# Optimization experiments

Hardware: AMD Instinct MI355X
Metric: run time of the kernel (lower is better)

Reference implementation:

```python
import jax, jax.numpy as jnp
import numpy as np

N = 50000        # nodes
E = 800000       # edges (avg degree 16)
OBS = 128        # observation_dim
HID = 64         # hidden_dim (per head)
H1 = 4           # heads in conv1
ACT = 32         # action_dim
NEG_SLOPE = 0.2  # GATv2 default negative_slope


def setup_inputs() -> dict:
    key = jax.random.key(0)
    ks = jax.random.split(key, 10)
    s = 0.05
    x = jax.random.normal(ks[0], (N, OBS), jnp.float32)
    edge_index = jax.random.randint(ks[1], (2, E), 0, N, dtype=jnp.int32)
    # conv1: GATv2Conv(OBS -> HID, heads=4, concat=True)
    W1l = jax.random.normal(ks[2], (OBS, H1 * HID), jnp.float32) * s  # lin_l (source)
    W1r = jax.random.normal(ks[3], (OBS, H1 * HID), jnp.float32) * s  # lin_r (target)
    att1 = jax.random.normal(ks[4], (H1, HID), jnp.float32) * s
    b1 = jnp.zeros((H1 * HID,), jnp.float32)
    # conv2: GATv2Conv(H1*HID -> ACT, heads=1, concat=False)
    W2l = jax.random.normal(ks[5], (H1 * HID, ACT), jnp.float32) * s
    W2r = jax.random.normal(ks[6], (H1 * HID, ACT), jnp.float32) * s
    att2 = jax.random.normal(ks[7], (1, ACT), jnp.float32) * s
    b2 = jnp.zeros((ACT,), jnp.float32)
    return {"x": x, "edge_index": edge_index, "W1l": W1l, "W1r": W1r,
            "att1": att1, "b1": b1, "W2l": W2l, "W2r": W2r,
            "att2": att2, "b2": b2}


def gatv2_layer(x, Wl, Wr, att, bias, src, dst, heads, out_ch, concat):
    """PyG GATv2Conv (add_self_loops=False, share_weights=False)."""
    n = x.shape[0]
    xl = (x @ Wl).reshape(n, heads, out_ch)  # source transform
    xr = (x @ Wr).reshape(n, heads, out_ch)  # target transform
    e = xl[src] + xr[dst]                    # [E, H, C] gathered messages
    g = jnp.where(e > 0, e, NEG_SLOPE * e)   # LeakyReLU
    logits = jnp.einsum('ehc,hc->eh', g, att)  # [E, H]
    # segment softmax over incoming edges of each destination node
    m = jax.ops.segment_max(logits, dst, num_segments=n)      # [N, H]
    ex = jnp.exp(logits - m[dst])
    denom = jax.ops.segment_sum(ex, dst, num_segments=n)      # [N, H]
    alpha = ex / denom[dst]                                   # [E, H]
    out = jax.ops.segment_sum(xl[src] * alpha[:, :, None], dst, num_segments=n)
    out = out.reshape(n, heads * out_ch) if concat else out.mean(axis=1)
    return out + bias


def reference(x, edge_index, W1l, W1r, att1, b1, W2l, W2r, att2, b2):
    src, dst = edge_index[0], edge_index[1]
    h = jax.nn.relu(gatv2_layer(x, W1l, W1r, att1, b1, src, dst, H1, HID, True))
    out = gatv2_layer(h, W2l, W2r, att2, b2, src, dst, 1, ACT, False)
    return out
```

## Files before the change

### kernel.cpp

```cpp
#include <hip/hip_runtime.h>
#include <hip/hip_bf16.h>
#include <math.h>


#define OBS 128
#define HID 64
#define H1 4
#define C1 256
#define ACT 32
#define PAD 128
#define NEG_SLOPE 0.2f
#define LOG2E 1.4426950408889634f

typedef __attribute__((ext_vector_type(2))) _Float16 h2;
typedef __attribute__((ext_vector_type(8))) _Float16 half8;
typedef __attribute__((ext_vector_type(4))) float f32x4;

__device__ inline h2 bc_h2(unsigned u) { return __builtin_bit_cast(h2, u); }
__device__ inline unsigned bc_u(h2 v) { return __builtin_bit_cast(unsigned, v); }
__device__ inline h2 lrelu2(h2 e) {
  const h2 k = {(_Float16)NEG_SLOPE, (_Float16)NEG_SLOPE};
  return __builtin_elementwise_max(e, e * k);
}

__global__ void prep0(const float* __restrict__ W1l, const float* __restrict__ W1r,
                      const float* __restrict__ W2l, const float* __restrict__ W2r,
                      _Float16* __restrict__ W1t, _Float16* __restrict__ W2t,
                      int* __restrict__ cursor, int N) {
  int i = blockIdx.x * 256 + threadIdx.x;
  if (i < N) cursor[i] = 0;
  if (i < 512 * 128) {
    int n = i >> 7, k = i & 127;
    float v = (n < C1) ? W1l[k * C1 + n] : W1r[k * C1 + (n - C1)];
    W1t[i] = (_Float16)v;
  }
  int j = i - 512 * 128;
  if (j >= 0 && j < 64 * 256) {
    int n = j >> 8, c = j & 255;
    float v = (n < ACT) ? W2l[c * ACT + n] : W2r[c * ACT + (n - ACT)];
    W2t[j] = (_Float16)v;
  }
}

__global__ __launch_bounds__(256) void gemm1_csr(
    const float* __restrict__ xf,
    const _Float16* __restrict__ W1t,
    _Float16* __restrict__ XLh,
    _Float16* __restrict__ XRh,
    int M,
    const int* __restrict__ src, const int* __restrict__ dst,
    int* __restrict__ cursor, unsigned short* __restrict__ esrc_p,
    int E, int gemmBlocks) {
  const int LDK = 136;
  __shared__ _Float16 As[128 * 136];
  __shared__ _Float16 Bs[128 * 136];

  if ((int)blockIdx.x >= gemmBlocks) {
    int e = ((int)blockIdx.x - gemmBlocks) * 256 + threadIdx.x;
    if (e < E) {
      int d = dst[e];
      int slot = atomicAdd(&cursor[d], 1);
      if (slot < PAD) esrc_p[((size_t)d << 7) + slot] = (unsigned short)src[e];
    }
    return;
  }

  const int tid = threadIdx.x;
  const int lane = tid & 63;
  const int wid = tid >> 6;
  const int wm = (wid & 1) * 64, wn = (wid >> 1) * 64;
  const int rowBase = blockIdx.x * 128;
  const int l15 = lane & 15, lq = lane >> 4;

#pragma unroll
  for (int cc = 0; cc < 8; ++cc) {
    int q = cc * 256 + tid;
    int r = q >> 4;
    int kc = (q & 15) * 8;
    int grow = rowBase + r;
    float4 f0 = make_float4(0.f, 0.f, 0.f, 0.f), f1 = f0;
    if (grow < M) {
      f0 = *(const float4*)(xf + (size_t)grow * 128 + kc);
      f1 = *(const float4*)(xf + (size_t)grow * 128 + kc + 4);
    }
    h2 p0 = {(_Float16)f0.x, (_Float16)f0.y};
    h2 p1 = {(_Float16)f0.z, (_Float16)f0.w};
    h2 p2 = {(_Float16)f1.x, (_Float16)f1.y};
    h2 p3 = {(_Float16)f1.z, (_Float16)f1.w};
    *(int4*)(As + r * LDK + kc) = make_int4(bc_u(p0), bc_u(p1), bc_u(p2), bc_u(p3));
  }
#pragma unroll
  for (int cc = 0; cc < 8; ++cc) {
    int q = cc * 256 + tid;
    int r = q >> 4;
    int kc = (q & 15) * 8;
    *(int4*)(Bs + r * LDK + kc) = *(const int4*)(W1t + (size_t)r * 128 + kc);
  }
  __syncthreads();

  for (int cb = 0; cb < 4; ++cb) {
    f32x4 acc[4][4];
#pragma unroll
    for (int i = 0; i < 4; ++i)
#pragma unroll
      for (int j = 0; j < 4; ++j) acc[i][j] = (f32x4){0.f, 0.f, 0.f, 0.f};

#pragma unroll
    for (int ks = 0; ks < 4; ++ks) {
      half8 af[4], bf[4];
#pragma unroll
      for (int t = 0; t < 4; ++t) {
        af[t] = *(const half8*)(As + (wm + t * 16 + l15) * LDK + ks * 32 + lq * 8);
        bf[t] = *(const half8*)(Bs + (wn + t * 16 + l15) * LDK + ks * 32 + lq * 8);
      }
#pragma unroll
      for (int mt = 0; mt < 4; ++mt)
#pragma unroll
        for (int nt = 0; nt < 4; ++nt)
          acc[mt][nt] = __builtin_amdgcn_mfma_f32_16x16x32_f16(
              af[mt], bf[nt], acc[mt][nt], 0, 0, 0);
    }

    _Float16* outp = (cb < 2) ? XLh : XRh;
    int colBase = (cb & 1) * 128;
#pragma unroll
    for (int mt = 0; mt < 4; ++mt) {
#pragma unroll
      for (int r = 0; r < 4; ++r) {
        int row = rowBase + wm + mt * 16 + lq * 4 + r;
        if (row >= M) continue;
#pragma unroll
        for (int nt = 0; nt < 4; ++nt) {
          int col = colBase + wn + nt * 16 + l15;
          outp[(size_t)row * C1 + col] = (_Float16)acc[mt][nt][r];
        }
      }
    }

    if (cb < 3) {
      __syncthreads();
#pragma unroll
      for (int cc = 0; cc < 8; ++cc) {
        int q = cc * 256 + tid;
        int r = q >> 4;
        int kc = (q & 15) * 8;
        *(int4*)(Bs + r * LDK + kc) =
            *(const int4*)(W1t + (size_t)((cb + 1) * 128 + r) * 128 + kc);
      }
      __syncthreads();
    }
  }
}

__global__ __launch_bounds__(256) void gemm_mfma2(
    const _Float16* __restrict__ Hh,
    const _Float16* __restrict__ W2t,
    _Float16* __restrict__ H2h,
    int M) {
  const int LDK = 136;
  __shared__ _Float16 As[128 * 136];
  __shared__ _Float16 Bs[64 * 136];
  const int tid = threadIdx.x;
  const int lane = tid & 63;
  const int wid = tid >> 6;
  const int wm = (wid & 1) * 64, wn = (wid >> 1) * 32;
  const int rowBase = blockIdx.x * 128;

  f32x4 acc[4][2];
#pragma unroll
  for (int i = 0; i < 4; ++i)
#pragma unroll
    for (int j = 0; j < 2; ++j) acc[i][j] = (f32x4){0.f, 0.f, 0.f, 0.f};

  const int l15 = lane & 15, lq = lane >> 4;

  for (int kb = 0; kb < 256; kb += 128) {
#pragma unroll
    for (int cc = 0; cc < 8; ++cc) {
      int q = cc * 256 + tid;
      int r = q >> 4;
      int kc = (q & 15) * 8;
      int grow = rowBase + r;
      int4 av = make_int4(0, 0, 0, 0);
      if (grow < M) av = *(const int4*)(Hh + (size_t)grow * 256 + kb + kc);
      *(int4*)(As + r * LDK + kc) = av;
    }
#pragma unroll
    for (int cc = 0; cc < 4; ++cc) {
      int q = cc * 256 + tid;
      int r = q >> 4;
      int kc = (q & 15) * 8;
      *(int4*)(Bs + r * LDK + kc) = *(const int4*)(W2t + (size_t)r * 256 + kb + kc);
    }
    __syncthreads();

#pragma unroll
    for (int ks = 0; ks < 4; ++ks) {
      half8 af[4], bf[2];
#pragma unroll
      for (int t = 0; t < 4; ++t)
        af[t] = *(const half8*)(As + (wm + t * 16 + l15) * LDK + ks * 32 + lq * 8);
#pragma unroll
      for (int t = 0; t < 2; ++t)
        bf[t] = *(const half8*)(Bs + (wn + t * 16 + l15) * LDK + ks * 32 + lq * 8);
#pragma unroll
      for (int mt = 0; mt < 4; ++mt)
#pragma unroll
        for (int nt = 0; nt < 2; ++nt)
          acc[mt][nt] = __builtin_amdgcn_mfma_f32_16x16x32_f16(
              af[mt], bf[nt], acc[mt][nt], 0, 0, 0);
    }
    __syncthreads();
  }

#pragma unroll
  for (int mt = 0; mt < 4; ++mt) {
#pragma unroll
    for (int r = 0; r < 4; ++r) {
      int row = rowBase + wm + mt * 16 + lq * 4 + r;
      if (row >= M) continue;
#pragma unroll
      for (int nt = 0; nt < 2; ++nt) {
        int col = wn + nt * 16 + l15;
        H2h[(size_t)row * 64 + col] = (_Float16)acc[mt][nt][r];
      }
    }
  }
}

__global__ __launch_bounds__(256) void agg1(const _Float16* __restrict__ XLh,
                                            const _Float16* XRh,
                                            const float* __restrict__ att1,
                                            const float* __restrict__ b1,
                                            const int* __restrict__ degp,
                                            const unsigned short* __restrict__ esrc_p,
                                            _Float16* Hh, int n_nodes) {
  int wave = threadIdx.x >> 6;
  int lane = threadIdx.x & 63;
  int n = blockIdx.x * 4 + wave;
  if (n >= n_nodes) return;
  int sl = lane & 31;
  int half = lane >> 5;
  int c8 = sl * 8;

  const char* XLb = (const char*)XLh + c8 * 2;
  int4 xru = *(const int4*)((const char*)XRh + ((size_t)n << 9) + c8 * 2);
  h2 xr[4] = {bc_h2(xru.x), bc_h2(xru.y), bc_h2(xru.z), bc_h2(xru.w)};
  const float* ap = att1 + (c8 >> 6) * HID + (c8 & 63);
  float4 a0 = *(const float4*)ap;
  float4 a1 = *(const float4*)(ap + 4);
  h2 av[4] = {{(_Float16)(a0.x * LOG2E), (_Float16)(a0.y * LOG2E)},
              {(_Float16)(a0.z * LOG2E), (_Float16)(a0.w * LOG2E)},
              {(_Float16)(a1.x * LOG2E), (_Float16)(a1.y * LOG2E)},
              {(_Float16)(a1.z * LOG2E), (_Float16)(a1.w * LOG2E)}};

  int d = min(degp[n], PAD);
  const unsigned short* ep = esrc_p + ((size_t)n << 7);
  float l = 0.f;
  h2 acc[4];
#pragma unroll
  for (int k = 0; k < 4; ++k) acc[k] = (h2){(_Float16)0.f, (_Float16)0.f};

  int base = 0;
  for (; base + 16 <= d; base += 16) {
    int4 u[8];
#pragma unroll
    for (int t = 0; t < 8; ++t) {
      int s = ep[base + 2 * t + half];
      u[t] = *(const int4*)(XLb + ((size_t)s << 9));
    }
    float c[8];
#pragma unroll
    for (int t = 0; t < 8; ++t) {
      h2 xa = bc_h2(u[t].x), xb = bc_h2(u[t].y), xc = bc_h2(u[t].z), xd = bc_h2(u[t].w);
      float cc = __builtin_amdgcn_fdot2(lrelu2(xa + xr[0]), av[0], 0.f, false);
      cc = __builtin_amdgcn_fdot2(lrelu2(xb + xr[1]), av[1], cc, false);
      cc = __builtin_amdgcn_fdot2(lrelu2(xc + xr[2]), av[2], cc, false);
      cc = __builtin_amdgcn_fdot2(lrelu2(xd + xr[3]), av[3], cc, false);
      c[t] = cc;
    }
#pragma unroll
    for (int t = 0; t < 8; ++t) {
      c[t] += __shfl_xor(c[t], 1);
      c[t] += __shfl_xor(c[t], 2);
      c[t] += __shfl_xor(c[t], 4);
    }
#pragma unroll
    for (int t = 0; t < 8; ++t) {
      float p = __builtin_amdgcn_exp2f(c[t]);
      l += p;
      _Float16 ph = (_Float16)p;
      h2 w = {ph, ph};
      acc[0] = acc[0] + w * bc_h2(u[t].x);
      acc[1] = acc[1] + w * bc_h2(u[t].y);
      acc[2] = acc[2] + w * bc_h2(u[t].z);
      acc[3] = acc[3] + w * bc_h2(u[t].w);
    }
  }
  for (; base + 4 <= d; base += 4) {
    int s0 = ep[base + half];
    int s1 = ep[base + 2 + half];
    int4 u0 = *(const int4*)(XLb + ((size_t)s0 << 9));
    int4 u1 = *(const int4*)(XLb + ((size_t)s1 << 9));
    h2 x0[4] = {bc_h2(u0.x), bc_h2(u0.y), bc_h2(u0.z), bc_h2(u0.w)};
    h2 x1[4] = {bc_h2(u1.x), bc_h2(u1.y), bc_h2(u1.z), bc_h2(u1.w)};
    float c0 = 0.f, c1 = 0.f;
#pragma unroll
    for (int k = 0; k < 4; ++k) {
      c0 = __builtin_amdgcn_fdot2(lrelu2(x0[k] + xr[k]), av[k], c0, false);
      c1 = __builtin_amdgcn_fdot2(lrelu2(x1[k] + xr[k]), av[k], c1, false);
    }
    c0 += __shfl_xor(c0, 1); c1 += __shfl_xor(c1, 1);
    c0 += __shfl_xor(c0, 2); c1 += __shfl_xor(c1, 2);
    c0 += __shfl_xor(c0, 4); c1 += __shfl_xor(c1, 4);
    float p0 = __builtin_amdgcn_exp2f(c0);
    float p1 = __builtin_amdgcn_exp2f(c1);
    l += p0 + p1;
    _Float16 q0 = (_Float16)p0, q1 = (_Float16)p1;
    h2 w0 = {q0, q0}, w1 = {q1, q1};
#pragma unroll
    for (int k = 0; k < 4; ++k) acc[k] = acc[k] + w0 * x0[k] + w1 * x1[k];
  }
  if (base < d) {
    int e0 = base + half, e1 = base + 2 + half;
    bool v0 = e0 < d, v1 = e1 < d;
    int s0 = ep[v0 ? e0 : 0];
    int s1 = ep[v1 ? e1 : 0];
    int4 u0 = *(const int4*)(XLb + ((size_t)s0 << 9));
    int4 u1 = *(const int4*)(XLb + ((size_t)s1 << 9));
    h2 x0[4] = {bc_h2(u0.x), bc_h2(u0.y), bc_h2(u0.z), bc_h2(u0.w)};
    h2 x1[4] = {bc_h2(u1.x), bc_h2(u1.y), bc_h2(u1.z), bc_h2(u1.w)};
    float c0 = 0.f, c1 = 0.f;
#pragma unroll
    for (int k = 0; k < 4; ++k) {
      c0 = __builtin_amdgcn_fdot2(lrelu2(x0[k] + xr[k]), av[k], c0, false);
      c1 = __builtin_amdgcn_fdot2(lrelu2(x1[k] + xr[k]), av[k], c1, false);
    }
    c0 += __shfl_xor(c0, 1); c1 += __shfl_xor(c1, 1);
    c0 += __shfl_xor(c0, 2); c1 += __shfl_xor(c1, 2);
    c0 += __shfl_xor(c0, 4); c1 += __shfl_xor(c1, 4);
    float p0 = v0 ? __builtin_amdgcn_exp2f(c0) : 0.f;
    float p1 = v1 ? __builtin_amdgcn_exp2f(c1) : 0.f;
    l += p0 + p1;
    _Float16 q0 = (_Float16)p0, q1 = (_Float16)p1;
    h2 w0 = {q0, q0}, w1 = {q1, q1};
#pragma unroll
    for (int k = 0; k < 4; ++k) acc[k] = acc[k] + w0 * x0[k] + w1 * x1[k];
  }

  l += __shfl_xor(l, 32);
#pragma unroll
  for (int k = 0; k < 4; ++k) {
    unsigned o = __shfl_xor((int)bc_u(acc[k]), 32);
    acc[k] = acc[k] + bc_h2(o);
  }

  float inv = (d > 0) ? 1.f / l : 0.f;
  if (half == 0) {
    float4 b0 = *(const float4*)(b1 + c8);
    float4 b3 = *(const float4*)(b1 + c8 + 4);
    float o0 = fmaxf((float)acc[0][0] * inv + b0.x, 0.f);
    float o1 = fmaxf((float)acc[0][1] * inv + b0.y, 0.f);
    float o2 = fmaxf((float)acc[1][0] * inv + b0.z, 0.f);
    float o3 = fmaxf((float)acc[1][1] * inv + b0.w, 0.f);
    float o4 = fmaxf((float)acc[2][0] * inv + b3.x, 0.f);
    float o5 = fmaxf((float)acc[2][1] * inv + b3.y, 0.f);
    float o6 = fmaxf((float)acc[3][0] * inv + b3.z, 0.f);
    float o7 = fmaxf((float)acc[3][1] * inv + b3.w, 0.f);
    h2 q0 = {(_Float16)o0, (_Float16)o1};
    h2 q1 = {(_Float16)o2, (_Float16)o3};
    h2 q2 = {(_Float16)o4, (_Float16)o5};
    h2 q3 = {(_Float16)o6, (_Float16)o7};
    *(int4*)((char*)Hh + ((size_t)n << 9) + c8 * 2) =
        make_int4(bc_u(q0), bc_u(q1), bc_u(q2), bc_u(q3));
  }
}

__global__ __launch_bounds__(256) void agg2(const _Float16* __restrict__ H2h,
                                            const float* __restrict__ att2,
                                            const float* __restrict__ b2,
                                            const int* __restrict__ degp,
                                            const unsigned short* __restrict__ esrc_p,
                                            float* __restrict__ out, int n_nodes) {
  int wave = threadIdx.x >> 6;
  int lane = threadIdx.x & 63;
  int n = blockIdx.x * 4 + wave;
  if (n >= n_nodes) return;
  int g = lane >> 3;
  int j = lane & 7;
  int c4 = j * 4;

  const char* Hb = (const char*)H2h + c4 * 2;
  uint2 hru = *(const uint2*)((const char*)H2h + ((size_t)n << 7) + 64 + c4 * 2);
  h2 hr0 = bc_h2(hru.x), hr1 = bc_h2(hru.y);
  float4 af = *(const float4*)(att2 + c4);
  h2 a0 = {(_Float16)(af.x * LOG2E), (_Float16)(af.y * LOG2E)};
  h2 a1 = {(_Float16)(af.z * LOG2E), (_Float16)(af.w * LOG2E)};

  int d = min(degp[n], PAD);
  const unsigned short* ep = esrc_p + ((size_t)n << 7);
  float l = 0.f;
  h2 acc0 = {(_Float16)0.f, (_Float16)0.f}, acc1 = acc0;

  int base = 0;
  for (; base + 16 <= d; base += 16) {
    int s0 = ep[base + g];
    int s1 = ep[base + 8 + g];
    uint2 u0 = *(const uint2*)(Hb + ((size_t)s0 << 7));
    uint2 u1 = *(const uint2*)(Hb + ((size_t)s1 << 7));
    h2 h00 = bc_h2(u0.x), h01 = bc_h2(u0.y);
    h2 h10 = bc_h2(u1.x), h11 = bc_h2(u1.y);
    float c0 = __builtin_amdgcn_fdot2(lrelu2(h00 + hr0), a0,
               __builtin_amdgcn_fdot2(lrelu2(h01 + hr1), a1, 0.f, false), false);
    float c1 = __builtin_amdgcn_fdot2(lrelu2(h10 + hr0), a0,
               __builtin_amdgcn_fdot2(lrelu2(h11 + hr1), a1, 0.f, false), false);
    c0 += __shfl_xor(c0, 1); c1 += __shfl_xor(c1, 1);
    c0 += __shfl_xor(c0, 2); c1 += __shfl_xor(c1, 2);
    c0 += __shfl_xor(c0, 4); c1 += __shfl_xor(c1, 4);
    float p0 = __builtin_amdgcn_exp2f(c0);
    float p1 = __builtin_amdgcn_exp2f(c1);
    l += p0 + p1;
    _Float16 q0 = (_Float16)p0, q1 = (_Float16)p1;
    h2 w0 = {q0, q0}, w1 = {q1, q1};
    acc0 = acc0 + w0 * h00 + w1 * h10;
    acc1 = acc1 + w0 * h01 + w1 * h11;
  }
  for (; base + 8 <= d; base += 8) {
    int s = ep[base + g];
    uint2 u = *(const uint2*)(Hb + ((size_t)s << 7));
    h2 h0 = bc_h2(u.x), h1 = bc_h2(u.y);
    float c = __builtin_amdgcn_fdot2(lrelu2(h0 + hr0), a0,
              __builtin_amdgcn_fdot2(lrelu2(h1 + hr1), a1, 0.f, false), false);
    c += __shfl_xor(c, 1);
    c += __shfl_xor(c, 2);
    c += __shfl_xor(c, 4);
    float p = __builtin_amdgcn_exp2f(c);
    l += p;
    _Float16 ph = (_Float16)p;
    h2 p2 = {ph, ph};
    acc0 = acc0 + p2 * h0;
    acc1 = acc1 + p2 * h1;
  }
  if (base < d) {
    int e = base + g;
    bool v = e < d;
    int s = ep[v ? e : 0];
    uint2 u = *(const uint2*)(Hb + ((size_t)s << 7));
    h2 h0 = bc_h2(u.x), h1 = bc_h2(u.y);
    float c = __builtin_amdgcn_fdot2(lrelu2(h0 + hr0), a0,
              __builtin_amdgcn_fdot2(lrelu2(h1 + hr1), a1, 0.f, false), false);
    c += __shfl_xor(c, 1);
    c += __shfl_xor(c, 2);
    c += __shfl_xor(c, 4);
    float p = v ? __builtin_amdgcn_exp2f(c) : 0.f;
    l += p;
    _Float16 ph = (_Float16)p;
    h2 p2 = {ph, ph};
    acc0 = acc0 + p2 * h0;
    acc1 = acc1 + p2 * h1;
  }

#pragma unroll
  for (int o = 8; o < 64; o <<= 1) {
    l += __shfl_xor(l, o);
    acc0 = acc0 + bc_h2((unsigned)__shfl_xor((int)bc_u(acc0), o));
    acc1 = acc1 + bc_h2((unsigned)__shfl_xor((int)bc_u(acc1), o));
  }

  float inv = (d > 0) ? 1.f / l : 0.f;
  if (g == 0) {
    float4 bb = *(const float4*)(b2 + c4);
    float4 o;
    o.x = (float)acc0[0] * inv + bb.x;
    o.y = (float)acc0[1] * inv + bb.y;
    o.z = (float)acc1[0] * inv + bb.z;
    o.w = (float)acc1[1] * inv + bb.w;
    *(float4*)(out + (size_t)n * ACT + c4) = o;
  }
}

extern "C" void kernel_launch(void* const* d_in, const int* in_sizes, int n_in,
                              void* d_out, int out_size, void* d_ws, size_t ws_size,
                              hipStream_t stream) {
  (void)n_in; (void)out_size; (void)ws_size;
  const float* x    = (const float*)d_in[0];
  const int*   ei   = (const int*)d_in[1];
  const float* W1l  = (const float*)d_in[2];
  const float* W1r  = (const float*)d_in[3];
  const float* att1 = (const float*)d_in[4];
  const float* b1   = (const float*)d_in[5];
  const float* W2l  = (const float*)d_in[6];
  const float* W2r  = (const float*)d_in[7];
  const float* att2 = (const float*)d_in[8];
  const float* b2   = (const float*)d_in[9];
  float* out = (float*)d_out;

  const int N = in_sizes[0] / OBS;
  const int E = in_sizes[1] / 2;
  const int* src = ei;
  const int* dst = ei + E;

  _Float16* XLh = (_Float16*)d_ws;
  _Float16* XRh = XLh + (size_t)N * C1;
  _Float16* W1t = XRh + (size_t)N * C1;
  _Float16* W2t = W1t + 512 * 128;
  int* cursor   = (int*)(W2t + 64 * 256);
  unsigned short* esrc_p = (unsigned short*)(cursor + N);
  _Float16* Hh  = XRh;
  _Float16* H2h = XLh;

  dim3 b256(256);
  int csrBlocks = (E + 255) / 256;
  int gemmBlocks = (N + 127) / 128;
  int prepBlocks = (512 * 128 + 64 * 256 + 255) / 256;

  prep0<<<prepBlocks, b256, 0, stream>>>(W1l, W1r, W2l, W2r, W1t, W2t, cursor, N);
  gemm1_csr<<<gemmBlocks + csrBlocks, b256, 0, stream>>>(
      x, W1t, XLh, XRh, N, src, dst, cursor, esrc_p, E, gemmBlocks);
  agg1<<<(N + 3) / 4, b256, 0, stream>>>(XLh, XRh, att1, b1, cursor, esrc_p, Hh, N);
  gemm_mfma2<<<gemmBlocks, b256, 0, stream>>>(Hh, W2t, H2h, N);
  agg2<<<(N + 3) / 4, b256, 0, stream>>>(H2h, att2, b2, cursor, esrc_p, out, N);
}
```

Before: 226.2 us.

## Build padded CSR via two-pass bucketed scatter instead of global atomics

Replaces the per-edge global atomicAdd on per-node cursors with a two-level bucket sort: edges are first scattered into 256-node buckets using shared-memory counts and one global atomic per bucket per block, then each bucket builds its padded neighbor lists with shared-memory atomics. This is meant to cut global atomic contention and scattered 2-byte writes. It also stops overlapping CSR construction with gemm1, adds two kernel launches, and places the sorted buffer at the start of the workspace, where it aliases XLh before gemm1 writes it. A bucket holding more than 8192 edges would overflow its region.

```diff
diff --git a/kernel.cpp b/kernel.cpp
--- a/kernel.cpp
+++ b/kernel.cpp
@@ -11,6 +11,8 @@
 #define PAD 128
 #define NEG_SLOPE 0.2f
 #define LOG2E 1.4426950408889634f
+#define SB 512
+#define CAP 8192
 
 typedef __attribute__((ext_vector_type(2))) _Float16 h2;
 typedef __attribute__((ext_vector_type(8))) _Float16 half8;
@@ -26,9 +28,9 @@
 __global__ void prep0(const float* __restrict__ W1l, const float* __restrict__ W1r,
                       const float* __restrict__ W2l, const float* __restrict__ W2r,
                       _Float16* __restrict__ W1t, _Float16* __restrict__ W2t,
-                      int* __restrict__ cursor, int N) {
+                      unsigned* __restrict__ bucketCursor) {
   int i = blockIdx.x * 256 + threadIdx.x;
-  if (i < N) cursor[i] = 0;
+  if (i < 256) bucketCursor[i] = 0;
   if (i < 512 * 128) {
     int n = i >> 7, k = i & 127;
     float v = (n < C1) ? W1l[k * C1 + n] : W1r[k * C1 + (n - C1)];
@@ -42,28 +44,70 @@
   }
 }
 
-__global__ __launch_bounds__(256) void gemm1_csr(
+__global__ __launch_bounds__(256) void scat2_k(const int* __restrict__ src,
+                                               const int* __restrict__ dst,
+                                               unsigned* __restrict__ bucketCursor,
+                                               unsigned* __restrict__ sorted,
+                                               int E, int epb) {
+  __shared__ unsigned cnt[256];
+  __shared__ unsigned lbase[256];
+  __shared__ unsigned lrank[256];
+  int t = threadIdx.x;
+  cnt[t] = 0;
+  lrank[t] = 0;
+  __syncthreads();
+  int beg = blockIdx.x * epb;
+  int end = beg + epb;
+  if (end > E) end = E;
+  for (int e = beg + t; e < end; e += 256)
+    atomicAdd(&cnt[dst[e] >> 8], 1u);
+  __syncthreads();
+  unsigned c = cnt[t];
+  lbase[t] = c ? atomicAdd(&bucketCursor[t], c) : 0u;
+  __syncthreads();
+  for (int e = beg + t; e < end; e += 256) {
+    int d = dst[e];
+    int sv = src[e];
+    int b = d >> 8;
+    unsigned r = atomicAdd(&lrank[b], 1u);
+    sorted[(size_t)b * CAP + lbase[b] + r] =
+        ((unsigned)(d & 255) << 16) | (unsigned)sv;
+  }
+}
+
+__global__ __launch_bounds__(256) void bcsr_k(const unsigned* __restrict__ sorted,
+                                              const unsigned* __restrict__ bucketCursor,
+                                              unsigned short* __restrict__ esrc_p,
+                                              int* __restrict__ cursor, int N) {
+  __shared__ unsigned cnt2[256];
+  int b = blockIdx.x;
+  int t = threadIdx.x;
+  cnt2[t] = 0;
+  __syncthreads();
+  unsigned total = bucketCursor[b];
+  const unsigned* sp = sorted + (size_t)b * CAP;
+  for (unsigned e = t; e < total; e += 256) {
+    unsigned u = sp[e];
+    unsigned dl = u >> 16;
+    unsigned slot = atomicAdd(&cnt2[dl], 1u);
+    if (slot < PAD)
+      esrc_p[((size_t)((b << 8) + (int)dl) << 7) + slot] =
+          (unsigned short)(u & 0xFFFFu);
+  }
+  __syncthreads();
+  int node = (b << 8) + t;
+  if (node < N) cursor[node] = (int)cnt2[t];
+}
+
+__global__ __launch_bounds__(256) void gemm1(
     const float* __restrict__ xf,
     const _Float16* __restrict__ W1t,
     _Float16* __restrict__ XLh,
     _Float16* __restrict__ XRh,
-    int M,
-    const int* __restrict__ src, const int* __restrict__ dst,
-    int* __restrict__ cursor, unsigned short* __restrict__ esrc_p,
-    int E, int gemmBlocks) {
+    int M) {
   const int LDK = 136;
   __shared__ _Float16 As[128 * 136];
   __shared__ _Float16 Bs[128 * 136];
-
-  if ((int)blockIdx.x >= gemmBlocks) {
-    int e = ((int)blockIdx.x - gemmBlocks) * 256 + threadIdx.x;
-    if (e < E) {
-      int d = dst[e];
-      int slot = atomicAdd(&cursor[d], 1);
-      if (slot < PAD) esrc_p[((size_t)d << 7) + slot] = (unsigned short)src[e];
-    }
-    return;
-  }
 
   const int tid = threadIdx.x;
   const int lane = tid & 63;
@@ -509,14 +553,19 @@
   _Float16* Hh  = XRh;
   _Float16* H2h = XLh;
 
+  unsigned* sortedW = (unsigned*)d_ws;
+  unsigned* bcur    = sortedW + 256 * CAP;
+
   dim3 b256(256);
-  int csrBlocks = (E + 255) / 256;
   int gemmBlocks = (N + 127) / 128;
   int prepBlocks = (512 * 128 + 64 * 256 + 255) / 256;
-
-  prep0<<<prepBlocks, b256, 0, stream>>>(W1l, W1r, W2l, W2r, W1t, W2t, cursor, N);
-  gemm1_csr<<<gemmBlocks + csrBlocks, b256, 0, stream>>>(
-      x, W1t, XLh, XRh, N, src, dst, cursor, esrc_p, E, gemmBlocks);
+  int NB = (N + 255) >> 8;
+  int epb = (E + SB - 1) / SB;
+
+  prep0<<<prepBlocks, b256, 0, stream>>>(W1l, W1r, W2l, W2r, W1t, W2t, bcur);
+  scat2_k<<<SB, b256, 0, stream>>>(src, dst, bcur, sortedW, E, epb);
+  bcsr_k<<<NB, b256, 0, stream>>>(sortedW, bcur, esrc_p, cursor, N);
+  gemm1<<<gemmBlocks, b256, 0, stream>>>(x, W1t, XLh, XRh, N);
   agg1<<<(N + 3) / 4, b256, 0, stream>>>(XLh, XRh, att1, b1, cursor, esrc_p, Hh, N);
   gemm_mfma2<<<gemmBlocks, b256, 0, stream>>>(Hh, W2t, H2h, N);
   agg2<<<(N + 3) / 4, b256, 0, stream>>>(H2h, att2, b2, cursor, esrc_p, out, N);
```

Measured after the change: 226.8 us. About the same (+0.2%).
